# Kernel optimization log

Measured on AMD Instinct MI355X. Metric: run time of the kernel, lower is better.

## Reference

```python
import jax, jax.numpy as jnp
import numpy as np

B, R, D = 64, 4, 768
H = W = 37
ROI_SIDE = 5


def setup_inputs() -> dict:
    key = jax.random.key(0)
    k1, k2, k3 = jax.random.split(key, 3)
    return {
        "cls_tok": jax.random.normal(k1, (B, D), dtype=jnp.float32),
        "regs": jax.random.normal(k2, (B, R, D), dtype=jnp.float32),
        "patches2d": jax.random.normal(k3, (B, H, W, D), dtype=jnp.float32),
        "roi_side": ROI_SIDE,
    }


def reference(cls_tok, regs, patches2d, roi_side):
    # cues: [B, C, d] with C = 1 + n_registers
    cues = jnp.concatenate([cls_tok[:, None, :], regs], axis=1)
    b, h_dim, w_dim, d = patches2d.shape
    r = roi_side // 2

    # similarity of every cue against every patch: [B, C, H, W]
    sim = jnp.einsum('bcd,bhwd->bchw', cues, patches2d)
    idx = jnp.argmax(sim.reshape(b, cues.shape[1], h_dim * w_dim), axis=-1)  # [B, C]
    hh = idx // w_dim
    ww = idx % w_dim

    # clipped window slice [max(0,h-r), min(H,h+r+1)) == rows with |row-h| <= r
    rows = jnp.arange(h_dim)
    cols = jnp.arange(w_dim)
    rmask = jnp.abs(rows[None, None, :] - hh[:, :, None]) <= r  # [B, C, H]
    cmask = jnp.abs(cols[None, None, :] - ww[:, :, None]) <= r  # [B, C, W]
    mask = (rmask[:, :, :, None] & cmask[:, :, None, :]).astype(patches2d.dtype)  # [B,C,H,W]

    num = jnp.einsum('bchw,bhwd->bcd', mask, patches2d)
    cnt = jnp.sum(mask, axis=(2, 3))  # [B, C]
    rois = num / cnt[:, :, None]      # mean over the (clipped) ROI window

    toks = jnp.concatenate([cues, rois], axis=1)  # [B, 2C, d]
    nrm = jnp.maximum(jnp.linalg.norm(toks, axis=-1, keepdims=True), 1e-12)
    return toks / nrm
```

## Files before the change

kernel.cpp:

```cpp
#include <hip/hip_runtime.h>
#include <hip/hip_bf16.h>

#define NB   64
#define NREG 4
#define ND   768
#define NH   37
#define NW   37
#define NC   5
#define NP   (NH * NW)
#define BPB  16
#define PPB  ((NP + BPB - 1) / BPB)
#define NWAVE 4
#define DEPTH 2

__device__ __forceinline__ unsigned int ord_of(float f) {
    unsigned int u = __float_as_uint(f);
    return (u & 0x80000000u) ? ~u : (u | 0x80000000u);
}

template <int CTRL>
__device__ __forceinline__ float dpp_add_step(float x) {
    int y = __builtin_amdgcn_update_dpp(0, __float_as_int(x), CTRL, 0xf, 0xf, true);
    return x + __int_as_float(y);
}
__device__ __forceinline__ float wave_sum_lane63(float x) {
    x = dpp_add_step<0x111>(x);
    x = dpp_add_step<0x112>(x);
    x = dpp_add_step<0x114>(x);
    x = dpp_add_step<0x118>(x);
    x = dpp_add_step<0x142>(x);
    x = dpp_add_step<0x143>(x);
    return x;
}

__device__ __forceinline__ void stage_patch(const float* __restrict__ gbase,
                                            float* lslot, int lane) {
    const float* g = gbase + lane * 4;
    #pragma unroll
    for (int k = 0; k < 3; ++k) {
        __builtin_amdgcn_global_load_lds(
            (const __attribute__((address_space(1))) void*)(g + k * 256),
            (__attribute__((address_space(3))) void*)(lslot + k * 256),
            16, 0, 0);
    }
}

__global__ __launch_bounds__(256, 4) void sim_argmax_kernel(
    const float* __restrict__ cls_tok,
    const float* __restrict__ regs,
    const float* __restrict__ patches,
    unsigned long long* __restrict__ pkeys)
{
    const int b    = blockIdx.x / BPB;
    const int pb   = blockIdx.x % BPB;
    const int wave = threadIdx.x >> 6;
    const int lane = threadIdx.x & 63;

    __shared__ float lds[DEPTH][NWAVE][ND];

    float4 cue[NC][3];
    #pragma unroll
    for (int c = 0; c < NC; ++c) {
        const float* cb = (c == 0) ? (cls_tok + (size_t)b * ND)
                                   : (regs + ((size_t)b * NREG + (c - 1)) * ND);
        #pragma unroll
        for (int k = 0; k < 3; ++k)
            cue[c][k] = *reinterpret_cast<const float4*>(cb + k * 256 + lane * 4);
    }

    float best[NC];
    int   bidx[NC];
    #pragma unroll
    for (int c = 0; c < NC; ++c) { best[c] = -3.4e38f; bidx[c] = 0; }

    const int pstart = pb * PPB;
    const int p1     = min(NP, pstart + PPB);
    const size_t bb  = (size_t)b * NP;
    const int p0     = pstart + wave;

    #pragma unroll
    for (int s = 0; s < DEPTH; ++s) {
        const int pp = p0 + s * NWAVE;
        if (pp < p1) stage_patch(patches + (bb + pp) * ND, &lds[s][wave][0], lane);
    }

    int it = 0;
    for (int pp = p0; pp < p1; pp += NWAVE, ++it) {
        const int s = it & 1;
        const bool more = (pp + NWAVE) < p1;

        if (more) asm volatile("s_waitcnt vmcnt(3)" ::: "memory");
        else      asm volatile("s_waitcnt vmcnt(0)" ::: "memory");

        const float* l = &lds[s][wave][0] + lane * 4;
        const float4 v0 = *reinterpret_cast<const float4*>(l);
        const float4 v1 = *reinterpret_cast<const float4*>(l + 256);
        const float4 v2 = *reinterpret_cast<const float4*>(l + 512);

        asm volatile("s_waitcnt lgkmcnt(0)" ::: "memory");

        const int pf = pp + DEPTH * NWAVE;
        if (pf < p1) stage_patch(patches + (bb + pf) * ND, &lds[s][wave][0], lane);

        float sacc[NC];
        #pragma unroll
        for (int c = 0; c < NC; ++c) {
            sacc[c] = v0.x * cue[c][0].x + v0.y * cue[c][0].y
                    + v0.z * cue[c][0].z + v0.w * cue[c][0].w
                    + v1.x * cue[c][1].x + v1.y * cue[c][1].y
                    + v1.z * cue[c][1].z + v1.w * cue[c][1].w
                    + v2.x * cue[c][2].x + v2.y * cue[c][2].y
                    + v2.z * cue[c][2].z + v2.w * cue[c][2].w;
        }
        #pragma unroll
        for (int c = 0; c < NC; ++c) {
            const float t = wave_sum_lane63(sacc[c]);
            if (t > best[c]) { best[c] = t; bidx[c] = pp; }
        }
    }

    __shared__ unsigned long long lk[NWAVE][NC];
    if (lane == 63) {
        #pragma unroll
        for (int c = 0; c < NC; ++c) {
            lk[wave][c] =
                ((unsigned long long)ord_of(best[c]) << 32) |
                (unsigned long long)(unsigned)(NP - 1 - bidx[c]);
        }
    }
    __syncthreads();
    if (threadIdx.x < NC) {
        unsigned long long k = lk[0][threadIdx.x];
        k = max(k, lk[1][threadIdx.x]);
        k = max(k, lk[2][threadIdx.x]);
        k = max(k, lk[3][threadIdx.x]);
        pkeys[(b * NC + threadIdx.x) * BPB + pb] = k;
    }
}

__global__ __launch_bounds__(192) void roi_norm_kernel(
    const float* __restrict__ cls_tok,
    const float* __restrict__ regs,
    const float* __restrict__ patches,
    const unsigned long long* __restrict__ pkeys,
    const int* __restrict__ roi_side_p,
    float* __restrict__ out)
{
    const int b   = blockIdx.x / NC;
    const int c   = blockIdx.x % NC;
    const int tid = threadIdx.x;
    const int wave = tid >> 6, lane = tid & 63;
    const int r = roi_side_p[0] >> 1;

    const unsigned long long* pk = pkeys + (b * NC + c) * BPB;
    unsigned long long key = pk[0];
    #pragma unroll
    for (int i = 1; i < BPB; ++i) key = max(key, pk[i]);

    const int idx = NP - 1 - (int)(key & 0xFFFFFFFFu);
    const int hh = idx / NW, ww = idx % NW;
    const int h0 = max(0, hh - r), h1 = min(NH - 1, hh + r);
    const int w0 = max(0, ww - r), w1 = min(NW - 1, ww + r);
    const float inv_cnt = 1.0f / (float)((h1 - h0 + 1) * (w1 - w0 + 1));

    const size_t bb = (size_t)b * NP;
    float4 acc = make_float4(0.f, 0.f, 0.f, 0.f);

    if (r == 2) {
        #pragma unroll
        for (int dh = -2; dh <= 2; ++dh) {
            #pragma unroll
            for (int dw = -2; dw <= 2; ++dw) {
                const int h = hh + dh, w = ww + dw;
                const bool ok = ((unsigned)h < NH) && ((unsigned)w < NW);
                const int pidx = ok ? (h * NW + w) : idx;
                const float m = ok ? 1.0f : 0.0f;
                const float4 v = *reinterpret_cast<const float4*>(
                    patches + (bb + pidx) * ND + tid * 4);
                acc.x += v.x * m; acc.y += v.y * m;
                acc.z += v.z * m; acc.w += v.w * m;
            }
        }
    } else {
        for (int h = h0; h <= h1; ++h) {
            for (int w = w0; w <= w1; ++w) {
                const float4 v = *reinterpret_cast<const float4*>(
                    patches + (bb + h * NW + w) * ND + tid * 4);
                acc.x += v.x; acc.y += v.y; acc.z += v.z; acc.w += v.w;
            }
        }
    }
    acc.x *= inv_cnt; acc.y *= inv_cnt; acc.z *= inv_cnt; acc.w *= inv_cnt;

    const float* cb = (c == 0) ? (cls_tok + (size_t)b * ND)
                               : (regs + ((size_t)b * NREG + (c - 1)) * ND);
    const float4 v = *reinterpret_cast<const float4*>(cb + tid * 4);

    float sx = v.x * v.x + v.y * v.y + v.z * v.z + v.w * v.w;
    float sy = acc.x * acc.x + acc.y * acc.y + acc.z * acc.z + acc.w * acc.w;
    #pragma unroll
    for (int off = 32; off > 0; off >>= 1) {
        sx += __shfl_xor(sx, off, 64);
        sy += __shfl_xor(sy, off, 64);
    }
    __shared__ float red_x[3], red_y[3];
    if (lane == 0) { red_x[wave] = sx; red_y[wave] = sy; }
    __syncthreads();
    const float tot_x = red_x[0] + red_x[1] + red_x[2];
    const float tot_y = red_y[0] + red_y[1] + red_y[2];
    const float inv_nc = 1.0f / fmaxf(sqrtf(tot_x), 1e-12f);
    const float inv_nr = 1.0f / fmaxf(sqrtf(tot_y), 1e-12f);

    float4* oc = reinterpret_cast<float4*>(out + ((size_t)b * 2 * NC + c) * ND) + tid;
    float4* om = reinterpret_cast<float4*>(out + ((size_t)b * 2 * NC + NC + c) * ND) + tid;
    *oc = make_float4(v.x * inv_nc, v.y * inv_nc, v.z * inv_nc, v.w * inv_nc);
    *om = make_float4(acc.x * inv_nr, acc.y * inv_nr, acc.z * inv_nr, acc.w * inv_nr);
}

extern "C" void kernel_launch(void* const* d_in, const int* in_sizes, int n_in,
                              void* d_out, int out_size, void* d_ws, size_t ws_size,
                              hipStream_t stream) {
    const float* cls_tok = (const float*)d_in[0];
    const float* regs    = (const float*)d_in[1];
    const float* patches = (const float*)d_in[2];
    const int*   roi     = (const int*)d_in[3];
    float* out = (float*)d_out;
    unsigned long long* pkeys = (unsigned long long*)d_ws;

    sim_argmax_kernel<<<NB * BPB, 256, 0, stream>>>(cls_tok, regs, patches, pkeys);
    roi_norm_kernel<<<NB * NC, 192, 0, stream>>>(cls_tok, regs, patches, pkeys, roi, out);
}
```

Measured before the change: 53.24 us.

## Fuse similarity-argmax and ROI-normalize kernels with per-batch atomic counters

Merges the two kernels into one launch. ROI blocks spin on a per-batch atomic counter until all 16 similarity blocks for that batch have published their argmax keys, then gather the window and normalize. The aim is to remove the kernel boundary and let ROI work overlap the tail of the similarity pass. It adds a memset launch, spin-waiting blocks that hold CU slots, and a recomputation of the ROI accumulation after the reduction. Correctness depends on ROI blocks not being scheduled ahead of, and starving, the producer blocks they wait on.

```diff
diff --git a/kernel.cpp b/kernel.cpp
--- a/kernel.cpp
+++ b/kernel.cpp
@@ -12,6 +12,8 @@
 #define PPB  ((NP + BPB - 1) / BPB)
 #define NWAVE 4
 #define DEPTH 2
+#define SIM_BLOCKS (NB * BPB)
+#define ROI_BLOCKS (NB * NC)
 
 __device__ __forceinline__ unsigned int ord_of(float f) {
     unsigned int u = __float_as_uint(f);
@@ -45,176 +47,224 @@
     }
 }
 
-__global__ __launch_bounds__(256, 4) void sim_argmax_kernel(
+__global__ __launch_bounds__(256, 4) void fused_encoder_kernel(
     const float* __restrict__ cls_tok,
     const float* __restrict__ regs,
     const float* __restrict__ patches,
-    unsigned long long* __restrict__ pkeys)
+    const int* __restrict__ roi_side_p,
+    float* __restrict__ out,
+    unsigned long long* __restrict__ pkeys,
+    unsigned int* __restrict__ cnt)
 {
-    const int b    = blockIdx.x / BPB;
-    const int pb   = blockIdx.x % BPB;
-    const int wave = threadIdx.x >> 6;
-    const int lane = threadIdx.x & 63;
+    const int tid  = threadIdx.x;
+    const int wave = tid >> 6;
+    const int lane = tid & 63;
 
     __shared__ float lds[DEPTH][NWAVE][ND];
-
-    float4 cue[NC][3];
-    #pragma unroll
-    for (int c = 0; c < NC; ++c) {
-        const float* cb = (c == 0) ? (cls_tok + (size_t)b * ND)
-                                   : (regs + ((size_t)b * NREG + (c - 1)) * ND);
-        #pragma unroll
-        for (int k = 0; k < 3; ++k)
-            cue[c][k] = *reinterpret_cast<const float4*>(cb + k * 256 + lane * 4);
-    }
-
-    float best[NC];
-    int   bidx[NC];
-    #pragma unroll
-    for (int c = 0; c < NC; ++c) { best[c] = -3.4e38f; bidx[c] = 0; }
-
-    const int pstart = pb * PPB;
-    const int p1     = min(NP, pstart + PPB);
-    const size_t bb  = (size_t)b * NP;
-    const int p0     = pstart + wave;
-
-    #pragma unroll
-    for (int s = 0; s < DEPTH; ++s) {
-        const int pp = p0 + s * NWAVE;
-        if (pp < p1) stage_patch(patches + (bb + pp) * ND, &lds[s][wave][0], lane);
-    }
-
-    int it = 0;
-    for (int pp = p0; pp < p1; pp += NWAVE, ++it) {
-        const int s = it & 1;
-        const bool more = (pp + NWAVE) < p1;
-
-        if (more) asm volatile("s_waitcnt vmcnt(3)" ::: "memory");
-        else      asm volatile("s_waitcnt vmcnt(0)" ::: "memory");
-
-        const float* l = &lds[s][wave][0] + lane * 4;
-        const float4 v0 = *reinterpret_cast<const float4*>(l);
-        const float4 v1 = *reinterpret_cast<const float4*>(l + 256);
-        const float4 v2 = *reinterpret_cast<const float4*>(l + 512);
-
-        asm volatile("s_waitcnt lgkmcnt(0)" ::: "memory");
-
-        const int pf = pp + DEPTH * NWAVE;
-        if (pf < p1) stage_patch(patches + (bb + pf) * ND, &lds[s][wave][0], lane);
-
-        float sacc[NC];
+    __shared__ unsigned long long lk[NWAVE][NC];
+    __shared__ unsigned long long skey;
+    __shared__ float red_x[3], red_y[3];
+
+    if (blockIdx.x < SIM_BLOCKS) {
+        const int b  = blockIdx.x / BPB;
+        const int pb = blockIdx.x % BPB;
+
+        float4 cue[NC][3];
         #pragma unroll
         for (int c = 0; c < NC; ++c) {
-            sacc[c] = v0.x * cue[c][0].x + v0.y * cue[c][0].y
-                    + v0.z * cue[c][0].z + v0.w * cue[c][0].w
-                    + v1.x * cue[c][1].x + v1.y * cue[c][1].y
-                    + v1.z * cue[c][1].z + v1.w * cue[c][1].w
-                    + v2.x * cue[c][2].x + v2.y * cue[c][2].y
-                    + v2.z * cue[c][2].z + v2.w * cue[c][2].w;
-        }
+            const float* cb = (c == 0) ? (cls_tok + (size_t)b * ND)
+                                       : (regs + ((size_t)b * NREG + (c - 1)) * ND);
+            #pragma unroll
+            for (int k = 0; k < 3; ++k)
+                cue[c][k] = *reinterpret_cast<const float4*>(cb + k * 256 + lane * 4);
+        }
+
+        float best[NC];
+        int   bidx[NC];
         #pragma unroll
-        for (int c = 0; c < NC; ++c) {
-            const float t = wave_sum_lane63(sacc[c]);
-            if (t > best[c]) { best[c] = t; bidx[c] = pp; }
+        for (int c = 0; c < NC; ++c) { best[c] = -3.4e38f; bidx[c] = 0; }
+
+        const int pstart = pb * PPB;
+        const int p1     = min(NP, pstart + PPB);
+        const size_t bb  = (size_t)b * NP;
+        const int p0     = pstart + wave;
+
+        #pragma unroll
+        for (int s = 0; s < DEPTH; ++s) {
+            const int pp = p0 + s * NWAVE;
+            if (pp < p1) stage_patch(patches + (bb + pp) * ND, &lds[s][wave][0], lane);
+        }
+
+        int it = 0;
+        for (int pp = p0; pp < p1; pp += NWAVE, ++it) {
+            const int s = it & 1;
+            const bool more = (pp + NWAVE) < p1;
+
+            if (more) asm volatile("s_waitcnt vmcnt(3)" ::: "memory");
+            else      asm volatile("s_waitcnt vmcnt(0)" ::: "memory");
+
+            const float* l = &lds[s][wave][0] + lane * 4;
+            const float4 v0 = *reinterpret_cast<const float4*>(l);
+            const float4 v1 = *reinterpret_cast<const float4*>(l + 256);
+            const float4 v2 = *reinterpret_cast<const float4*>(l + 512);
+
+            asm volatile("s_waitcnt lgkmcnt(0)" ::: "memory");
+
+            const int pf = pp + DEPTH * NWAVE;
+            if (pf < p1) stage_patch(patches + (bb + pf) * ND, &lds[s][wave][0], lane);
+
+            float sacc[NC];
+            #pragma unroll
+            for (int c = 0; c < NC; ++c) {
+                sacc[c] = v0.x * cue[c][0].x + v0.y * cue[c][0].y
+                        + v0.z * cue[c][0].z + v0.w * cue[c][0].w
+                        + v1.x * cue[c][1].x + v1.y * cue[c][1].y
+                        + v1.z * cue[c][1].z + v1.w * cue[c][1].w
+                        + v2.x * cue[c][2].x + v2.y * cue[c][2].y
+                        + v2.z * cue[c][2].z + v2.w * cue[c][2].w;
+            }
+            #pragma unroll
+            for (int c = 0; c < NC; ++c) {
+                const float t = wave_sum_lane63(sacc[c]);
+                if (t > best[c]) { best[c] = t; bidx[c] = pp; }
+            }
+        }
+
+        if (lane == 63) {
+            #pragma unroll
+            for (int c = 0; c < NC; ++c) {
+                lk[wave][c] =
+                    ((unsigned long long)ord_of(best[c]) << 32) |
+                    (unsigned long long)(unsigned)(NP - 1 - bidx[c]);
+            }
+        }
+        __syncthreads();
+        if (tid < NC) {
+            unsigned long long k = lk[0][tid];
+            k = max(k, lk[1][tid]);
+            k = max(k, lk[2][tid]);
+            k = max(k, lk[3][tid]);
+            atomicExch(&pkeys[(b * NC + tid) * BPB + pb], k);
+        }
+        __syncthreads();
+        if (tid == 0) {
+            __threadfence();
+            atomicAdd(&cnt[b], 1u);
+        }
+    } else {
+        const int rb = blockIdx.x - SIM_BLOCKS;
+        const int b  = rb / NC;
+        const int c  = rb % NC;
+
+        if (tid == 0) {
+            while (atomicAdd(&cnt[b], 0u) < BPB) __builtin_amdgcn_s_sleep(2);
+        }
+        __syncthreads();
+        __threadfence();
+
+        if (wave == 0) {
+            unsigned long long k = (lane < BPB)
+                ? atomicAdd(&pkeys[(b * NC + c) * BPB + lane], 0ull) : 0ull;
+            #pragma unroll
+            for (int off = 8; off > 0; off >>= 1) {
+                const unsigned long long o = __shfl_xor(k, off, 64);
+                k = max(k, o);
+            }
+            if (lane == 0) skey = k;
+        }
+        __syncthreads();
+        const unsigned long long key = skey;
+
+        const int r = roi_side_p[0] >> 1;
+        const int idx = NP - 1 - (int)(key & 0xFFFFFFFFu);
+        const int hh = idx / NW, ww = idx % NW;
+        const int h0 = max(0, hh - r), h1 = min(NH - 1, hh + r);
+        const int w0 = max(0, ww - r), w1 = min(NW - 1, ww + r);
+        const float inv_cnt = 1.0f / (float)((h1 - h0 + 1) * (w1 - w0 + 1));
+        const size_t bb = (size_t)b * NP;
+
+        if (tid < 192) {
+            float4 acc = make_float4(0.f, 0.f, 0.f, 0.f);
+            if (r == 2) {
+                #pragma unroll
+                for (int dh = -2; dh <= 2; ++dh) {
+                    #pragma unroll
+                    for (int dw = -2; dw <= 2; ++dw) {
+                        const int h = hh + dh, w = ww + dw;
+                        const bool ok = ((unsigned)h < NH) && ((unsigned)w < NW);
+                        const int pidx = ok ? (h * NW + w) : idx;
+                        const float m = ok ? 1.0f : 0.0f;
+                        const float4 v = *reinterpret_cast<const float4*>(
+                            patches + (bb + pidx) * ND + tid * 4);
+                        acc.x += v.x * m; acc.y += v.y * m;
+                        acc.z += v.z * m; acc.w += v.w * m;
+                    }
+                }
+            } else {
+                for (int h = h0; h <= h1; ++h)
+                    for (int w = w0; w <= w1; ++w) {
+                        const float4 v = *reinterpret_cast<const float4*>(
+                            patches + (bb + h * NW + w) * ND + tid * 4);
+                        acc.x += v.x; acc.y += v.y; acc.z += v.z; acc.w += v.w;
+                    }
+            }
+            acc.x *= inv_cnt; acc.y *= inv_cnt; acc.z *= inv_cnt; acc.w *= inv_cnt;
+
+            const float* cb = (c == 0) ? (cls_tok + (size_t)b * ND)
+                                       : (regs + ((size_t)b * NREG + (c - 1)) * ND);
+            const float4 v = *reinterpret_cast<const float4*>(cb + tid * 4);
+
+            float sx = v.x * v.x + v.y * v.y + v.z * v.z + v.w * v.w;
+            float sy = acc.x * acc.x + acc.y * acc.y + acc.z * acc.z + acc.w * acc.w;
+            #pragma unroll
+            for (int off = 32; off > 0; off >>= 1) {
+                sx += __shfl_xor(sx, off, 64);
+                sy += __shfl_xor(sy, off, 64);
+            }
+            if (lane == 0) { red_x[wave] = sx; red_y[wave] = sy; }
+        }
+        __syncthreads();
+        if (tid < 192) {
+            const float tot_x = red_x[0] + red_x[1] + red_x[2];
+            const float tot_y = red_y[0] + red_y[1] + red_y[2];
+            const float inv_nc = 1.0f / fmaxf(sqrtf(tot_x), 1e-12f);
+            const float inv_nr = 1.0f / fmaxf(sqrtf(tot_y), 1e-12f);
+
+            const float* cb = (c == 0) ? (cls_tok + (size_t)b * ND)
+                                       : (regs + ((size_t)b * NREG + (c - 1)) * ND);
+            const float4 v = *reinterpret_cast<const float4*>(cb + tid * 4);
+            float4 acc = make_float4(0.f, 0.f, 0.f, 0.f);
+            if (r == 2) {
+                #pragma unroll
+                for (int dh = -2; dh <= 2; ++dh) {
+                    #pragma unroll
+                    for (int dw = -2; dw <= 2; ++dw) {
+                        const int h = hh + dh, w = ww + dw;
+                        const bool ok = ((unsigned)h < NH) && ((unsigned)w < NW);
+                        const int pidx = ok ? (h * NW + w) : idx;
+                        const float m = ok ? 1.0f : 0.0f;
+                        const float4 t = *reinterpret_cast<const float4*>(
+                            patches + (bb + pidx) * ND + tid * 4);
+                        acc.x += t.x * m; acc.y += t.y * m;
+                        acc.z += t.z * m; acc.w += t.w * m;
+                    }
+                }
+            } else {
+                for (int h = h0; h <= h1; ++h)
+                    for (int w = w0; w <= w1; ++w) {
+                        const float4 t = *reinterpret_cast<const float4*>(
+                            patches + (bb + h * NW + w) * ND + tid * 4);
+                        acc.x += t.x; acc.y += t.y; acc.z += t.z; acc.w += t.w;
+                    }
+            }
+            acc.x *= inv_cnt; acc.y *= inv_cnt; acc.z *= inv_cnt; acc.w *= inv_cnt;
+
+            float4* oc = reinterpret_cast<float4*>(out + ((size_t)b * 2 * NC + c) * ND) + tid;
+            float4* om = reinterpret_cast<float4*>(out + ((size_t)b * 2 * NC + NC + c) * ND) + tid;
+            *oc = make_float4(v.x * inv_nc, v.y * inv_nc, v.z * inv_nc, v.w * inv_nc);
+            *om = make_float4(acc.x * inv_nr, acc.y * inv_nr, acc.z * inv_nr, acc.w * inv_nr);
         }
     }
-
-    __shared__ unsigned long long lk[NWAVE][NC];
-    if (lane == 63) {
-        #pragma unroll
-        for (int c = 0; c < NC; ++c) {
-            lk[wave][c] =
-                ((unsigned long long)ord_of(best[c]) << 32) |
-                (unsigned long long)(unsigned)(NP - 1 - bidx[c]);
-        }
-    }
-    __syncthreads();
-    if (threadIdx.x < NC) {
-        unsigned long long k = lk[0][threadIdx.x];
-        k = max(k, lk[1][threadIdx.x]);
-        k = max(k, lk[2][threadIdx.x]);
-        k = max(k, lk[3][threadIdx.x]);
-        pkeys[(b * NC + threadIdx.x) * BPB + pb] = k;
-    }
-}
-
-__global__ __launch_bounds__(192) void roi_norm_kernel(
-    const float* __restrict__ cls_tok,
-    const float* __restrict__ regs,
-    const float* __restrict__ patches,
-    const unsigned long long* __restrict__ pkeys,
-    const int* __restrict__ roi_side_p,
-    float* __restrict__ out)
-{
-    const int b   = blockIdx.x / NC;
-    const int c   = blockIdx.x % NC;
-    const int tid = threadIdx.x;
-    const int wave = tid >> 6, lane = tid & 63;
-    const int r = roi_side_p[0] >> 1;
-
-    const unsigned long long* pk = pkeys + (b * NC + c) * BPB;
-    unsigned long long key = pk[0];
-    #pragma unroll
-    for (int i = 1; i < BPB; ++i) key = max(key, pk[i]);
-
-    const int idx = NP - 1 - (int)(key & 0xFFFFFFFFu);
-    const int hh = idx / NW, ww = idx % NW;
-    const int h0 = max(0, hh - r), h1 = min(NH - 1, hh + r);
-    const int w0 = max(0, ww - r), w1 = min(NW - 1, ww + r);
-    const float inv_cnt = 1.0f / (float)((h1 - h0 + 1) * (w1 - w0 + 1));
-
-    const size_t bb = (size_t)b * NP;
-    float4 acc = make_float4(0.f, 0.f, 0.f, 0.f);
-
-    if (r == 2) {
-        #pragma unroll
-        for (int dh = -2; dh <= 2; ++dh) {
-            #pragma unroll
-            for (int dw = -2; dw <= 2; ++dw) {
-                const int h = hh + dh, w = ww + dw;
-                const bool ok = ((unsigned)h < NH) && ((unsigned)w < NW);
-                const int pidx = ok ? (h * NW + w) : idx;
-                const float m = ok ? 1.0f : 0.0f;
-                const float4 v = *reinterpret_cast<const float4*>(
-                    patches + (bb + pidx) * ND + tid * 4);
-                acc.x += v.x * m; acc.y += v.y * m;
-                acc.z += v.z * m; acc.w += v.w * m;
-            }
-        }
-    } else {
-        for (int h = h0; h <= h1; ++h) {
-            for (int w = w0; w <= w1; ++w) {
-                const float4 v = *reinterpret_cast<const float4*>(
-                    patches + (bb + h * NW + w) * ND + tid * 4);
-                acc.x += v.x; acc.y += v.y; acc.z += v.z; acc.w += v.w;
-            }
-        }
-    }
-    acc.x *= inv_cnt; acc.y *= inv_cnt; acc.z *= inv_cnt; acc.w *= inv_cnt;
-
-    const float* cb = (c == 0) ? (cls_tok + (size_t)b * ND)
-                               : (regs + ((size_t)b * NREG + (c - 1)) * ND);
-    const float4 v = *reinterpret_cast<const float4*>(cb + tid * 4);
-
-    float sx = v.x * v.x + v.y * v.y + v.z * v.z + v.w * v.w;
-    float sy = acc.x * acc.x + acc.y * acc.y + acc.z * acc.z + acc.w * acc.w;
-    #pragma unroll
-    for (int off = 32; off > 0; off >>= 1) {
-        sx += __shfl_xor(sx, off, 64);
-        sy += __shfl_xor(sy, off, 64);
-    }
-    __shared__ float red_x[3], red_y[3];
-    if (lane == 0) { red_x[wave] = sx; red_y[wave] = sy; }
-    __syncthreads();
-    const float tot_x = red_x[0] + red_x[1] + red_x[2];
-    const float tot_y = red_y[0] + red_y[1] + red_y[2];
-    const float inv_nc = 1.0f / fmaxf(sqrtf(tot_x), 1e-12f);
-    const float inv_nr = 1.0f / fmaxf(sqrtf(tot_y), 1e-12f);
-
-    float4* oc = reinterpret_cast<float4*>(out + ((size_t)b * 2 * NC + c) * ND) + tid;
-    float4* om = reinterpret_cast<float4*>(out + ((size_t)b * 2 * NC + NC + c) * ND) + tid;
-    *oc = make_float4(v.x * inv_nc, v.y * inv_nc, v.z * inv_nc, v.w * inv_nc);
-    *om = make_float4(acc.x * inv_nr, acc.y * inv_nr, acc.z * inv_nr, acc.w * inv_nr);
 }
 
 extern "C" void kernel_launch(void* const* d_in, const int* in_sizes, int n_in,
@@ -225,8 +275,13 @@
     const float* patches = (const float*)d_in[2];
     const int*   roi     = (const int*)d_in[3];
     float* out = (float*)d_out;
+
     unsigned long long* pkeys = (unsigned long long*)d_ws;
-
-    sim_argmax_kernel<<<NB * BPB, 256, 0, stream>>>(cls_tok, regs, patches, pkeys);
-    roi_norm_kernel<<<NB * NC, 192, 0, stream>>>(cls_tok, regs, patches, pkeys, roi, out);
-}
+    unsigned int* cnt = (unsigned int*)((char*)d_ws +
+                         (size_t)NB * NC * BPB * sizeof(unsigned long long));
+
+    hipMemsetAsync(cnt, 0, NB * sizeof(unsigned int), stream);
+
+    fused_encoder_kernel<<<SIM_BLOCKS + ROI_BLOCKS, 256, 0, stream>>>(
+        cls_tok, regs, patches, roi, out, pkeys, cnt);
+}
```

Result: slower. 171.9 us (+223.0%).
